# Kernel tuning notes

Hardware: AMD Instinct MI355X
Metric: run time of the kernel (lower is better)

## Reference

```python
import jax, jax.numpy as jnp
import numpy as np

B, S, D, H, M = 2, 2048, 1024, 16, 4096
DH = D // H
EPS = 1e-6  # flax LayerNorm default
THETA = 10000.0


def layer_norm(x, scale, bias):
    m = jnp.mean(x, axis=-1, keepdims=True)
    v = jnp.var(x, axis=-1, keepdims=True)
    return (x - m) * jax.lax.rsqrt(v + EPS) * scale + bias


def apply_rope(xq, xk):
    # xq, xk: [B, S, H, DH]; rotate consecutive pairs as complex numbers
    half = DH // 2
    freqs = 1.0 / THETA ** (jnp.arange(0, DH, 2)[:half].astype(jnp.float32) / DH)
    t = jnp.arange(S, dtype=jnp.float32)
    ang = jnp.outer(t, freqs)                      # [S, half]
    cos = jnp.cos(ang)[None, :, None, :]           # [1, S, 1, half]
    sin = jnp.sin(ang)[None, :, None, :]

    def rot(x):
        xr = x.astype(jnp.float32).reshape(*x.shape[:-1], half, 2)
        a, b = xr[..., 0], xr[..., 1]
        out = jnp.stack((a * cos - b * sin, a * sin + b * cos), axis=-1)
        return out.reshape(*x.shape).astype(jnp.float32)

    return rot(xq), rot(xk)


def setup_inputs() -> dict:
    key = jax.random.key(0)
    ks = jax.random.split(key, 12)
    sd = 1.0 / np.sqrt(D)
    return {
        "x": jax.random.normal(ks[0], (B, S, D), jnp.float32),
        "ln1_s": jnp.ones((D,), jnp.float32),
        "ln1_b": jnp.zeros((D,), jnp.float32),
        "wk": jax.random.normal(ks[1], (D, D), jnp.float32) * sd,
        "wq": jax.random.normal(ks[2], (D, D), jnp.float32) * sd,
        "wv": jax.random.normal(ks[3], (D, D), jnp.float32) * sd,
        "wo": jax.random.normal(ks[4], (D, D), jnp.float32) * sd,
        "ln2_s": jnp.ones((D,), jnp.float32),
        "ln2_b": jnp.zeros((D,), jnp.float32),
        "w1": jax.random.normal(ks[5], (D, M), jnp.float32) * sd,
        "b1": jnp.zeros((M,), jnp.float32),
        "w2": jax.random.normal(ks[6], (M, D), jnp.float32) * (1.0 / np.sqrt(M)),
        "b2": jnp.zeros((D,), jnp.float32),
    }


def reference(x, ln1_s, ln1_b, wk, wq, wv, wo, ln2_s, ln2_b, w1, b1, w2, b2):
    h = layer_norm(x, ln1_s, ln1_b)
    xk = (h @ wk).reshape(B, S, H, DH)
    xq = (h @ wq).reshape(B, S, H, DH)
    xv = (h @ wv).reshape(B, S, H, DH)
    xq, xk = apply_rope(xq, xk)
    # scores: [B, H, S, S]
    scores = jnp.einsum("bqhd,bkhd->bhqk", xq, xk) / jnp.sqrt(jnp.float32(DH))
    attn = jax.nn.softmax(scores, axis=-1)
    ctx = jnp.einsum("bhqk,bkhd->bqhd", attn, xv).reshape(B, S, D)
    attn_out = ctx @ wo
    mlp_in = attn_out + x
    h2 = layer_norm(mlp_in, ln2_s, ln2_b)
    h2 = jax.nn.gelu(h2 @ w1 + b1)  # approximate gelu (jax default, matches source)
    h2 = h2 @ w2 + b2
    return h2 + mlp_in
```

## Files before the change

kernel.cpp:

```cpp
#include <hip/hip_runtime.h>
#include <stdint.h>

#define B_ 2
#define S_ 2048
#define D_ 1024
#define H_ 16
#define DH_ 64
#define M_ 4096
#define BS_ 4096

typedef __attribute__((ext_vector_type(8))) short short8;
typedef __attribute__((ext_vector_type(4))) float f32x4;
typedef __attribute__((ext_vector_type(16))) float f32x16;

static __device__ __forceinline__ unsigned short f2bf(float f) {
  unsigned u = __float_as_uint(f);
  u += 0x7fffu + ((u >> 16) & 1u);
  return (unsigned short)(u >> 16);
}
static __device__ __forceinline__ float bf2f(unsigned short s) {
  return __uint_as_float(((unsigned)s) << 16);
}
static __device__ __forceinline__ f32x4 MFMA16(short8 a, short8 b, f32x4 c) {
  return __builtin_amdgcn_mfma_f32_16x16x32_bf16(a, b, c, 0, 0, 0);
}
static __device__ __forceinline__ f32x16 MFMA32(short8 a, short8 b, f32x16 c) {
  return __builtin_amdgcn_mfma_f32_32x32x16_bf16(a, b, c, 0, 0, 0);
}
static __device__ __forceinline__ void gload_lds16(const void* g, void* l) {
  __builtin_amdgcn_global_load_lds(
      (const __attribute__((address_space(1))) unsigned int*)g,
      (__attribute__((address_space(3))) unsigned int*)l, 16, 0, 0);
}
static __device__ __forceinline__ unsigned cvtpk_bf16(float lo, float hi) {
  unsigned r;
  asm("v_cvt_pk_bf16_f32 %0, %1, %2" : "=v"(r) : "v"(lo), "v"(hi));
  return r;
}
static __device__ __forceinline__ float gelu_f(float x) {
  float u = 0.7978845608028654f * (x + 0.044715f * x * x * x);
  return 0.5f * x * (1.0f + tanhf(u));
}

__global__ __launch_bounds__(256) void tcast_kernel(const float* __restrict__ in,
                                                    unsigned short* __restrict__ out,
                                                    int R, int C) {
  __shared__ float tile[32][33];
  int tx = threadIdx.x & 31, ty = threadIdx.x >> 5;
  int r0 = blockIdx.y * 32, c0 = blockIdx.x * 32;
#pragma unroll
  for (int i = 0; i < 4; ++i)
    tile[ty + i * 8][tx] = in[(size_t)(r0 + ty + i * 8) * C + c0 + tx];
  __syncthreads();
#pragma unroll
  for (int i = 0; i < 4; ++i)
    out[(size_t)(c0 + ty + i * 8) * R + r0 + tx] = f2bf(tile[tx][ty + i * 8]);
}

__global__ __launch_bounds__(256) void ln_kernel(const float* __restrict__ x,
                                                 const float* __restrict__ sc,
                                                 const float* __restrict__ bi,
                                                 unsigned short* __restrict__ out) {
  int row = blockIdx.x;
  int t = threadIdx.x;
  float4 v = ((const float4*)(x + (size_t)row * D_))[t];
  float s1 = v.x + v.y + v.z + v.w;
  float s2 = v.x * v.x + v.y * v.y + v.z * v.z + v.w * v.w;
#pragma unroll
  for (int m = 1; m < 64; m <<= 1) {
    s1 += __shfl_xor(s1, m);
    s2 += __shfl_xor(s2, m);
  }
  __shared__ float red[8];
  int w = t >> 6, l = t & 63;
  if (l == 0) { red[w] = s1; red[4 + w] = s2; }
  __syncthreads();
  s1 = red[0] + red[1] + red[2] + red[3];
  s2 = red[4] + red[5] + red[6] + red[7];
  float mean = s1 * (1.0f / D_);
  float var = s2 * (1.0f / D_) - mean * mean;
  float rstd = rsqrtf(var + 1e-6f);
  float4 scv = ((const float4*)sc)[t];
  float4 biv = ((const float4*)bi)[t];
  ushort4 o;
  o.x = f2bf((v.x - mean) * rstd * scv.x + biv.x);
  o.y = f2bf((v.y - mean) * rstd * scv.y + biv.y);
  o.z = f2bf((v.z - mean) * rstd * scv.z + biv.z);
  o.w = f2bf((v.w - mean) * rstd * scv.w + biv.w);
  ((ushort4*)out)[(size_t)row * (D_ / 4) + t] = o;
}

__global__ __launch_bounds__(256) void rope_kernel(unsigned short* __restrict__ t_,
                                                   float qscale) {
  size_t idx = (size_t)blockIdx.x * 256 + threadIdx.x;
  int c = (int)(idx & 7);
  size_t rowi = idx >> 3;
  int s = (int)(rowi & (S_ - 1));
  unsigned short* p = t_ + rowi * DH_ + c * 8;
  short8 v = *(const short8*)p;
  unsigned short o[8];
#pragma unroll
  for (int i = 0; i < 4; ++i) {
    int pi = c * 4 + i;
    float freq = exp2f(-(float)pi * 0.4152410118609203f);
    float ang = (float)s * freq;
    float sn, cs;
    sincosf(ang, &sn, &cs);
    float a = bf2f((unsigned short)v[2 * i]);
    float b = bf2f((unsigned short)v[2 * i + 1]);
    o[2 * i] = f2bf((a * cs - b * sn) * qscale);
    o[2 * i + 1] = f2bf((a * sn + b * cs) * qscale);
  }
  short8 ov;
#pragma unroll
  for (int i = 0; i < 8; ++i) ov[i] = (short)o[i];
  *(short8*)p = ov;
}

__global__ __launch_bounds__(256) void attn_kernel(const unsigned short* __restrict__ q,
                                                   const unsigned short* __restrict__ k,
                                                   const unsigned short* __restrict__ vt,
                                                   unsigned short* __restrict__ ctx) {
  __shared__ char smem[49152];
  const int tid = threadIdx.x, w = tid >> 6, l = tid & 63;
  const int lo = l & 31, hi = l >> 5;
  char* Ps = smem + 32768 + w * 4096;
  int flat = blockIdx.y * 16 + blockIdx.x;
  int swz = (flat & 7) * 64 + (flat >> 3);
  const int bh = swz >> 4;
  const int b = bh >> 4, h = bh & 15;
  const int q0 = (swz & 15) * 128 + w * 32;

  const unsigned short* qbase = q + ((size_t)bh * S_ + q0 + lo) * DH_ + hi * 8;
  short8 qf[4];
#pragma unroll
  for (int c = 0; c < 4; ++c) qf[c] = *(const short8*)(qbase + c * 16);

  const unsigned short* kb = k + (size_t)bh * S_ * DH_;
  const unsigned short* vb = vt + (size_t)bh * DH_ * S_;

  short8 onesB;
#pragma unroll
  for (int i = 0; i < 8; ++i) onesB[i] = (short)0x3F80;

  f32x16 o0, o1, lac;
#pragma unroll
  for (int i = 0; i < 16; ++i) { o0[i] = 0.f; o1[i] = 0.f; lac[i] = 0.f; }

#define STAGE_KV(buf, kt)                                                        \
  {                                                                              \
    char* Ks_ = smem + (buf) * 16384;                                            \
    char* Vs_ = Ks_ + 8192;                                                      \
    _Pragma("unroll") for (int i = 0; i < 2; ++i) {                              \
      int slot = i * 256 + tid;                                                  \
      int r = slot >> 3, pc = slot & 7;                                          \
      int sc_ = pc ^ (r & 7);                                                    \
      gload_lds16(kb + (size_t)((kt) + r) * DH_ + sc_ * 8,                       \
                  Ks_ + (i * 4096 + w * 1024));                                  \
      gload_lds16(vb + (size_t)r * S_ + (kt) + sc_ * 8,                          \
                  Vs_ + (i * 4096 + w * 1024));                                  \
    }                                                                            \
  }

  STAGE_KV(0, 0);
  asm volatile("s_waitcnt vmcnt(0)" ::: "memory");
  __builtin_amdgcn_s_barrier();

  for (int t = 0; t < S_ / 64; ++t) {
    int buf = t & 1;
    if (t + 1 < S_ / 64) STAGE_KV(buf ^ 1, (t + 1) * 64);
    char* Ks = smem + buf * 16384;
    char* Vs = Ks + 8192;

#pragma unroll
    for (int kt2 = 0; kt2 < 2; ++kt2) {
      f32x16 z;
#pragma unroll
      for (int i = 0; i < 16; ++i) z[i] = 0.f;
      __builtin_amdgcn_s_setprio(1);
#pragma unroll
      for (int c = 0; c < 4; ++c) {
        int r = kt2 * 32 + lo;
        short8 kf = *(const short8*)(Ks + r * 128 + (((hi + 2 * c) ^ (r & 7)) << 4));
        z = MFMA32(kf, qf[c], z);
      }
      __builtin_amdgcn_s_setprio(0);
      unsigned pk[8];
#pragma unroll
      for (int e = 0; e < 8; ++e)
        pk[e] = cvtpk_bf16(exp2f(z[2 * e]), exp2f(z[2 * e + 1]));
#pragma unroll
      for (int s2 = 0; s2 < 4; ++s2) {
        uint2 dd;
        dd.x = pk[2 * s2];
        dd.y = pk[2 * s2 + 1];
        int slot = kt2 * 4 + s2;
        *(uint2*)(Ps + lo * 128 + ((slot ^ (lo & 7)) << 4) + hi * 8) = dd;
      }
    }

    __builtin_amdgcn_s_setprio(1);
#pragma unroll
    for (int c = 0; c < 4; ++c) {
      short8 pa = *(const short8*)(Ps + lo * 128 + (((2 * c + hi) ^ (lo & 7)) << 4));
      lac = MFMA32(pa, onesB, lac);
      int r0v = lo, r1v = 32 + lo;
      short8 vf0 = *(const short8*)(Vs + r0v * 128 + (((2 * c + hi) ^ (r0v & 7)) << 4));
      short8 vf1 = *(const short8*)(Vs + r1v * 128 + (((2 * c + hi) ^ (r1v & 7)) << 4));
      o0 = MFMA32(pa, vf0, o0);
      o1 = MFMA32(pa, vf1, o1);
    }
    __builtin_amdgcn_s_setprio(0);
    asm volatile("s_waitcnt vmcnt(0)" ::: "memory");
    __builtin_amdgcn_s_barrier();
  }

#pragma unroll
  for (int r = 0; r < 16; ++r) {
    float rl = 1.0f / lac[r];
    int srow = q0 + (r & 3) + 8 * (r >> 2) + 4 * hi;
    unsigned short* cp = ctx + ((size_t)(b * S_) + srow) * D_ + h * DH_ + lo;
    cp[0] = f2bf(o0[r] * rl);
    cp[32] = f2bf(o1[r] * rl);
  }
#undef STAGE_KV
}

template <int EPI>
__global__ __launch_bounds__(256) void gemm_bt(const unsigned short* __restrict__ A,
                                               const unsigned short* __restrict__ Bt,
                                               int K,
                                               const float* __restrict__ aux0,
                                               const float* __restrict__ aux1,
                                               void* __restrict__ out0,
                                               void* __restrict__ out1,
                                               void* __restrict__ out2) {
  __shared__ char smem[65536];
  int tid = threadIdx.x, w = tid >> 6, l = tid & 63;
  int wr = w >> 1, wc = w & 1;
  int gx = gridDim.x;
  int nwg = gx * gridDim.y;
  int flat = blockIdx.y * gx + blockIdx.x;
  int swz = (flat & 7) * (nwg >> 3) + (flat >> 3);
  int row0 = (swz / gx) * 128, col0 = (swz % gx) * 128;
  f32x4 acc[4][4];
#pragma unroll
  for (int mt = 0; mt < 4; ++mt)
#pragma unroll
    for (int nt = 0; nt < 4; ++nt) {
      f32x4 z = {0.f, 0.f, 0.f, 0.f};
      acc[mt][nt] = z;
    }
  int lr = l >> 3, lc = l & 7;

#define STAGE_AB(buf, kt)                                                        \
  {                                                                              \
    char* As_ = smem + (buf) * 32768;                                            \
    char* Bs_ = As_ + 16384;                                                     \
    _Pragma("unroll") for (int i = 0; i < 4; ++i) {                              \
      int rb = w * 32 + i * 8;                                                   \
      int r = rb + lr;                                                           \
      int sc_ = lc ^ (r & 7);                                                    \
      gload_lds16(A + (size_t)(row0 + r) * K + (kt) + sc_ * 8, As_ + rb * 128);  \
      gload_lds16(Bt + (size_t)(col0 + r) * K + (kt) + sc_ * 8, Bs_ + rb * 128); \
    }                                                                            \
  }

  STAGE_AB(0, 0);
  asm volatile("s_waitcnt vmcnt(0)" ::: "memory");
  __builtin_amdgcn_s_barrier();

  const int NT = K >> 6;
  for (int t = 0; t < NT; ++t) {
    int buf = t & 1;
    if (t + 1 < NT) STAGE_AB(buf ^ 1, (t + 1) * 64);
    char* As = smem + buf * 32768;
    char* Bs = As + 16384;
#pragma unroll
    for (int kf = 0; kf < 2; ++kf) {
      short8 af[4], bfr[4];
#pragma unroll
      for (int mt = 0; mt < 4; ++mt) {
        int r = wr * 64 + mt * 16 + (l & 15);
        int c = (l >> 4) + 4 * kf;
        af[mt] = *(const short8*)(As + r * 128 + ((c ^ (r & 7)) << 4));
      }
#pragma unroll
      for (int nt = 0; nt < 4; ++nt) {
        int r = wc * 64 + nt * 16 + (l & 15);
        int c = (l >> 4) + 4 * kf;
        bfr[nt] = *(const short8*)(Bs + r * 128 + ((c ^ (r & 7)) << 4));
      }
#pragma unroll
      for (int mt = 0; mt < 4; ++mt)
#pragma unroll
        for (int nt = 0; nt < 4; ++nt)
          acc[mt][nt] = MFMA16(af[mt], bfr[nt], acc[mt][nt]);
    }
    asm volatile("s_waitcnt vmcnt(0)" ::: "memory");
    __builtin_amdgcn_s_barrier();
  }
#undef STAGE_AB

#pragma unroll
  for (int mt = 0; mt < 4; ++mt) {
#pragma unroll
    for (int nt = 0; nt < 4; ++nt) {
      int grow0 = row0 + wr * 64 + mt * 16 + ((l >> 4) << 2);
      int gcol = col0 + wc * 64 + nt * 16 + (l & 15);
      if (EPI == 0) {
        int which = gcol >> 10;
        int d = gcol & 1023;
        int hh = d >> 6, dh = d & 63;
#pragma unroll
        for (int r = 0; r < 4; ++r) {
          int grow = grow0 + r;
          int b = grow >> 11, s = grow & 2047;
          float v = acc[mt][nt][r];
          if (which == 0)
            ((unsigned short*)out0)[(((size_t)(b * H_ + hh)) * S_ + s) * DH_ + dh] = f2bf(v);
          else if (which == 1)
            ((unsigned short*)out1)[(((size_t)(b * H_ + hh)) * S_ + s) * DH_ + dh] = f2bf(v);
          else
            ((unsigned short*)out2)[(((size_t)(b * H_ + hh)) * DH_ + dh) * S_ + s] = f2bf(v);
        }
      } else if (EPI == 1) {
        float* mo = (float*)out0;
#pragma unroll
        for (int r = 0; r < 4; ++r) {
          int grow = grow0 + r;
          mo[(size_t)grow * D_ + gcol] = acc[mt][nt][r] + aux0[(size_t)grow * D_ + gcol];
        }
      } else if (EPI == 2) {
        unsigned short* gq = (unsigned short*)out0;
        float bb = aux0[gcol];
#pragma unroll
        for (int r = 0; r < 4; ++r) {
          int grow = grow0 + r;
          gq[(size_t)grow * M_ + gcol] = f2bf(gelu_f(acc[mt][nt][r] + bb));
        }
      } else {
        float* po = (float*)out0;
        float bb = aux0[gcol];
#pragma unroll
        for (int r = 0; r < 4; ++r) {
          int grow = grow0 + r;
          po[(size_t)grow * D_ + gcol] =
              acc[mt][nt][r] + bb + aux1[(size_t)grow * D_ + gcol];
        }
      }
    }
  }
}

extern "C" void kernel_launch(void* const* d_in, const int* in_sizes, int n_in,
                              void* d_out, int out_size, void* d_ws, size_t ws_size,
                              hipStream_t stream) {
  const float* x = (const float*)d_in[0];
  const float* ln1s = (const float*)d_in[1];
  const float* ln1b = (const float*)d_in[2];
  const float* wk = (const float*)d_in[3];
  const float* wq = (const float*)d_in[4];
  const float* wv = (const float*)d_in[5];
  const float* wo = (const float*)d_in[6];
  const float* ln2s = (const float*)d_in[7];
  const float* ln2b = (const float*)d_in[8];
  const float* w1 = (const float*)d_in[9];
  const float* b1 = (const float*)d_in[10];
  const float* w2 = (const float*)d_in[11];
  const float* b2 = (const float*)d_in[12];

  char* ws = (char*)d_ws;
  unsigned short* wqkv_t = (unsigned short*)(ws);
  unsigned short* wo_t = (unsigned short*)(ws + 6291456);
  unsigned short* w1_t = (unsigned short*)(ws + 8388608);
  unsigned short* w2_t = (unsigned short*)(ws + 16777216);
  unsigned short* h_bf = (unsigned short*)(ws + 25165824);
  unsigned short* q_bf = (unsigned short*)(ws + 33554432);
  unsigned short* k_bf = (unsigned short*)(ws + 41943040);
  unsigned short* vt_bf = (unsigned short*)(ws + 50331648);
  unsigned short* ctx_bf = (unsigned short*)(ws + 58720256);
  float* mlp_in = (float*)(ws + 67108864);
  unsigned short* g_bf = (unsigned short*)(ws + 83886080);

  dim3 blk(256);
  tcast_kernel<<<dim3(32, 32), blk, 0, stream>>>(wq, wqkv_t, 1024, 1024);
  tcast_kernel<<<dim3(32, 32), blk, 0, stream>>>(wk, wqkv_t + 1048576, 1024, 1024);
  tcast_kernel<<<dim3(32, 32), blk, 0, stream>>>(wv, wqkv_t + 2097152, 1024, 1024);
  tcast_kernel<<<dim3(32, 32), blk, 0, stream>>>(wo, wo_t, 1024, 1024);
  tcast_kernel<<<dim3(128, 32), blk, 0, stream>>>(w1, w1_t, 1024, 4096);
  tcast_kernel<<<dim3(32, 128), blk, 0, stream>>>(w2, w2_t, 4096, 1024);
  ln_kernel<<<dim3(BS_), blk, 0, stream>>>(x, ln1s, ln1b, h_bf);
  gemm_bt<0><<<dim3(24, 32), blk, 0, stream>>>(h_bf, wqkv_t, 1024, nullptr, nullptr,
                                               q_bf, k_bf, vt_bf);
  rope_kernel<<<dim3(2048), blk, 0, stream>>>(q_bf, 0.125f * 1.4426950408889634f);
  rope_kernel<<<dim3(2048), blk, 0, stream>>>(k_bf, 1.0f);
  attn_kernel<<<dim3(16, 32), blk, 0, stream>>>(q_bf, k_bf, vt_bf, ctx_bf);
  gemm_bt<1><<<dim3(8, 32), blk, 0, stream>>>(ctx_bf, wo_t, 1024, x, nullptr,
                                              mlp_in, nullptr, nullptr);
  ln_kernel<<<dim3(BS_), blk, 0, stream>>>(mlp_in, ln2s, ln2b, h_bf);
  gemm_bt<2><<<dim3(32, 32), blk, 0, stream>>>(h_bf, w1_t, 1024, b1, nullptr,
                                               g_bf, nullptr, nullptr);
  gemm_bt<3><<<dim3(8, 32), blk, 0, stream>>>(g_bf, w2_t, 4096, b2, mlp_in,
                                              (float*)d_out, nullptr, nullptr);
}
```

Measured before the change: 372.6 us.

## Split attention over key halves with register-resident P and combine kernel

Attention is restructured so each wave handles 64 query rows, reusing each K/V LDS fragment across two query tiles. The key range is split into two halves processed by separate blocks, and a new combine kernel merges them. The P matrix now stays in registers via v_permlane32_swap instead of round-tripping through LDS, and the ones-matrix MFMA row sum becomes scalar accumulation. The cost is partial outputs written and re-read through workspace in bf16, plus an extra launch; softmax still has no max subtraction, which is fine only for bounded scores.

```diff
diff --git a/kernel.cpp b/kernel.cpp
--- a/kernel.cpp
+++ b/kernel.cpp
@@ -36,6 +36,9 @@
   unsigned r;
   asm("v_cvt_pk_bf16_f32 %0, %1, %2" : "=v"(r) : "v"(lo), "v"(hi));
   return r;
+}
+static __device__ __forceinline__ void pl32swap(unsigned& a, unsigned& b) {
+  asm volatile("v_permlane32_swap_b32 %0, %1" : "+v"(a), "+v"(b));
 }
 static __device__ __forceinline__ float gelu_f(float x) {
   float u = 0.7978845608028654f * (x + 0.044715f * x * x * x);
@@ -117,35 +120,40 @@
   *(short8*)p = ov;
 }
 
-__global__ __launch_bounds__(256) void attn_kernel(const unsigned short* __restrict__ q,
-                                                   const unsigned short* __restrict__ k,
-                                                   const unsigned short* __restrict__ vt,
-                                                   unsigned short* __restrict__ ctx) {
-  __shared__ char smem[49152];
+__global__ __launch_bounds__(256, 2) void attn_part_kernel(
+    const unsigned short* __restrict__ q, const unsigned short* __restrict__ k,
+    const unsigned short* __restrict__ vt, unsigned short* __restrict__ po,
+    float* __restrict__ pl) {
+  __shared__ char smem[32768];
   const int tid = threadIdx.x, w = tid >> 6, l = tid & 63;
   const int lo = l & 31, hi = l >> 5;
-  char* Ps = smem + 32768 + w * 4096;
-  int flat = blockIdx.y * 16 + blockIdx.x;
-  int swz = (flat & 7) * 64 + (flat >> 3);
-  const int bh = swz >> 4;
+  int f = blockIdx.x;
+  int xcd = f & 7, within = f >> 3;
+  const int bh = xcd * 4 + (within >> 4);
+  int sub = within & 15;
+  const int qt = sub >> 1, ks = sub & 1;
   const int b = bh >> 4, h = bh & 15;
-  const int q0 = (swz & 15) * 128 + w * 32;
-
-  const unsigned short* qbase = q + ((size_t)bh * S_ + q0 + lo) * DH_ + hi * 8;
-  short8 qf[4];
-#pragma unroll
-  for (int c = 0; c < 4; ++c) qf[c] = *(const short8*)(qbase + c * 16);
+  const int qbase = qt * 256 + w * 64;
+  const int kbase = ks * 1024;
+
+  unsigned short* po_k = po + (size_t)ks * (B_ * S_ * D_);
+  float* pl_k = pl + (size_t)ks * (32 * S_);
+
+  const unsigned short* qb0 = q + ((size_t)bh * S_ + qbase + lo) * DH_ + hi * 8;
+  short8 qf0[4], qf1[4];
+#pragma unroll
+  for (int c = 0; c < 4; ++c) {
+    qf0[c] = *(const short8*)(qb0 + c * 16);
+    qf1[c] = *(const short8*)(qb0 + 32 * DH_ + c * 16);
+  }
 
   const unsigned short* kb = k + (size_t)bh * S_ * DH_;
   const unsigned short* vb = vt + (size_t)bh * DH_ * S_;
 
-  short8 onesB;
-#pragma unroll
-  for (int i = 0; i < 8; ++i) onesB[i] = (short)0x3F80;
-
-  f32x16 o0, o1, lac;
-#pragma unroll
-  for (int i = 0; i < 16; ++i) { o0[i] = 0.f; o1[i] = 0.f; lac[i] = 0.f; }
+  f32x16 o00, o01, o10, o11;
+#pragma unroll
+  for (int i = 0; i < 16; ++i) { o00[i] = 0.f; o01[i] = 0.f; o10[i] = 0.f; o11[i] = 0.f; }
+  float rs0 = 0.f, rs1 = 0.f;
 
 #define STAGE_KV(buf, kt)                                                        \
   {                                                                              \
@@ -162,68 +170,107 @@
     }                                                                            \
   }
 
-  STAGE_KV(0, 0);
+  STAGE_KV(0, kbase);
   asm volatile("s_waitcnt vmcnt(0)" ::: "memory");
   __builtin_amdgcn_s_barrier();
 
-  for (int t = 0; t < S_ / 64; ++t) {
+  for (int t = 0; t < 16; ++t) {
     int buf = t & 1;
-    if (t + 1 < S_ / 64) STAGE_KV(buf ^ 1, (t + 1) * 64);
+    if (t + 1 < 16) STAGE_KV(buf ^ 1, kbase + (t + 1) * 64);
     char* Ks = smem + buf * 16384;
     char* Vs = Ks + 8192;
 
+    unsigned pk0[16], pk1[16];
 #pragma unroll
     for (int kt2 = 0; kt2 < 2; ++kt2) {
-      f32x16 z;
-#pragma unroll
-      for (int i = 0; i < 16; ++i) z[i] = 0.f;
+      f32x16 z0, z1;
+#pragma unroll
+      for (int i = 0; i < 16; ++i) { z0[i] = 0.f; z1[i] = 0.f; }
       __builtin_amdgcn_s_setprio(1);
 #pragma unroll
       for (int c = 0; c < 4; ++c) {
         int r = kt2 * 32 + lo;
-        short8 kf = *(const short8*)(Ks + r * 128 + (((hi + 2 * c) ^ (r & 7)) << 4));
-        z = MFMA32(kf, qf[c], z);
+        short8 kf = *(const short8*)(Ks + r * 128 + (((2 * c + hi) ^ (r & 7)) << 4));
+        z0 = MFMA32(kf, qf0[c], z0);
+        z1 = MFMA32(kf, qf1[c], z1);
       }
       __builtin_amdgcn_s_setprio(0);
-      unsigned pk[8];
-#pragma unroll
-      for (int e = 0; e < 8; ++e)
-        pk[e] = cvtpk_bf16(exp2f(z[2 * e]), exp2f(z[2 * e + 1]));
-#pragma unroll
-      for (int s2 = 0; s2 < 4; ++s2) {
-        uint2 dd;
-        dd.x = pk[2 * s2];
-        dd.y = pk[2 * s2 + 1];
-        int slot = kt2 * 4 + s2;
-        *(uint2*)(Ps + lo * 128 + ((slot ^ (lo & 7)) << 4) + hi * 8) = dd;
+#pragma unroll
+      for (int e = 0; e < 8; ++e) {
+        float a0 = exp2f(z0[2 * e]), b0 = exp2f(z0[2 * e + 1]);
+        float a1 = exp2f(z1[2 * e]), b1 = exp2f(z1[2 * e + 1]);
+        rs0 += a0 + b0;
+        rs1 += a1 + b1;
+        pk0[kt2 * 8 + e] = cvtpk_bf16(a0, b0);
+        pk1[kt2 * 8 + e] = cvtpk_bf16(a1, b1);
       }
     }
 
     __builtin_amdgcn_s_setprio(1);
 #pragma unroll
-    for (int c = 0; c < 4; ++c) {
-      short8 pa = *(const short8*)(Ps + lo * 128 + (((2 * c + hi) ^ (lo & 7)) << 4));
-      lac = MFMA32(pa, onesB, lac);
+    for (int cc = 0; cc < 4; ++cc) {
+      const int base = (cc >> 1) * 8 + (cc & 1) * 4;
+      unsigned a0 = pk0[base + 0], c0 = pk0[base + 2];
+      pl32swap(a0, c0);
+      unsigned b0v = pk0[base + 1], d0v = pk0[base + 3];
+      pl32swap(b0v, d0v);
+      unsigned a1 = pk1[base + 0], c1 = pk1[base + 2];
+      pl32swap(a1, c1);
+      unsigned b1v = pk1[base + 1], d1v = pk1[base + 3];
+      pl32swap(b1v, d1v);
+      union { unsigned u[4]; short8 v; } pa0, pa1;
+      pa0.u[0] = a0; pa0.u[1] = b0v; pa0.u[2] = c0; pa0.u[3] = d0v;
+      pa1.u[0] = a1; pa1.u[1] = b1v; pa1.u[2] = c1; pa1.u[3] = d1v;
       int r0v = lo, r1v = 32 + lo;
-      short8 vf0 = *(const short8*)(Vs + r0v * 128 + (((2 * c + hi) ^ (r0v & 7)) << 4));
-      short8 vf1 = *(const short8*)(Vs + r1v * 128 + (((2 * c + hi) ^ (r1v & 7)) << 4));
-      o0 = MFMA32(pa, vf0, o0);
-      o1 = MFMA32(pa, vf1, o1);
+      short8 vf0 = *(const short8*)(Vs + r0v * 128 + (((2 * cc + hi) ^ (r0v & 7)) << 4));
+      short8 vf1 = *(const short8*)(Vs + r1v * 128 + (((2 * cc + hi) ^ (r1v & 7)) << 4));
+      o00 = MFMA32(pa0.v, vf0, o00);
+      o01 = MFMA32(pa0.v, vf1, o01);
+      o10 = MFMA32(pa1.v, vf0, o10);
+      o11 = MFMA32(pa1.v, vf1, o11);
     }
     __builtin_amdgcn_s_setprio(0);
     asm volatile("s_waitcnt vmcnt(0)" ::: "memory");
     __builtin_amdgcn_s_barrier();
   }
 
+  rs0 += __shfl_xor(rs0, 32);
+  rs1 += __shfl_xor(rs1, 32);
+  if (hi == 0) {
+    pl_k[(size_t)bh * S_ + qbase + lo] = rs0;
+    pl_k[(size_t)bh * S_ + qbase + 32 + lo] = rs1;
+  }
 #pragma unroll
   for (int r = 0; r < 16; ++r) {
-    float rl = 1.0f / lac[r];
-    int srow = q0 + (r & 3) + 8 * (r >> 2) + 4 * hi;
-    unsigned short* cp = ctx + ((size_t)(b * S_) + srow) * D_ + h * DH_ + lo;
-    cp[0] = f2bf(o0[r] * rl);
-    cp[32] = f2bf(o1[r] * rl);
+    int srow = qbase + (r & 3) + 8 * (r >> 2) + 4 * hi;
+    unsigned short* p0 = po_k + ((size_t)(b * S_) + srow) * D_ + h * DH_ + lo;
+    p0[0] = f2bf(o00[r]);
+    p0[32] = f2bf(o01[r]);
+    unsigned short* p1 = po_k + ((size_t)(b * S_) + srow + 32) * D_ + h * DH_ + lo;
+    p1[0] = f2bf(o10[r]);
+    p1[32] = f2bf(o11[r]);
   }
 #undef STAGE_KV
+}
+
+__global__ __launch_bounds__(256) void attn_combine_kernel(
+    const unsigned short* __restrict__ po, const float* __restrict__ pl,
+    unsigned short* __restrict__ ctx) {
+  size_t i8 = (size_t)blockIdx.x * 256 + threadIdx.x;
+  size_t i = i8 * 8;
+  int d = (int)(i & 1023);
+  int h = d >> 6;
+  int s = (int)((i >> 10) & 2047);
+  int b = (int)(i >> 21);
+  size_t lidx = ((size_t)(b * 16 + h)) * S_ + s;
+  float rl = 1.0f / (pl[lidx] + pl[(size_t)(32 * S_) + lidx]);
+  short8 a = *(const short8*)(po + i);
+  short8 c = *(const short8*)(po + (size_t)(B_ * S_ * D_) + i);
+  short8 o;
+#pragma unroll
+  for (int j = 0; j < 8; ++j)
+    o[j] = (short)f2bf((bf2f((unsigned short)a[j]) + bf2f((unsigned short)c[j])) * rl);
+  *(short8*)(ctx + i) = o;
 }
 
 template <int EPI>
@@ -383,6 +430,9 @@
   float* mlp_in = (float*)(ws + 67108864);
   unsigned short* g_bf = (unsigned short*)(ws + 83886080);
 
+  unsigned short* po = (unsigned short*)mlp_in;
+  float* pl = (float*)h_bf;
+
   dim3 blk(256);
   tcast_kernel<<<dim3(32, 32), blk, 0, stream>>>(wq, wqkv_t, 1024, 1024);
   tcast_kernel<<<dim3(32, 32), blk, 0, stream>>>(wk, wqkv_t + 1048576, 1024, 1024);
@@ -395,7 +445,8 @@
                                                q_bf, k_bf, vt_bf);
   rope_kernel<<<dim3(2048), blk, 0, stream>>>(q_bf, 0.125f * 1.4426950408889634f);
   rope_kernel<<<dim3(2048), blk, 0, stream>>>(k_bf, 1.0f);
-  attn_kernel<<<dim3(16, 32), blk, 0, stream>>>(q_bf, k_bf, vt_bf, ctx_bf);
+  attn_part_kernel<<<dim3(512), blk, 0, stream>>>(q_bf, k_bf, vt_bf, po, pl);
+  attn_combine_kernel<<<dim3(2048), blk, 0, stream>>>(po, pl, ctx_bf);
   gemm_bt<1><<<dim3(8, 32), blk, 0, stream>>>(ctx_bf, wo_t, 1024, x, nullptr,
                                               mlp_in, nullptr, nullptr);
   ln_kernel<<<dim3(BS_), blk, 0, stream>>>(mlp_in, ln2s, ln2b, h_bf);
```

Result: slower. 401.3 us (+7.7%).
